# Performance work log

Measured on AMD Instinct MI355X. Metric: run time of the kernel, lower is better.

The kernel has to match this reference:

```python
import jax, jax.numpy as jnp
import numpy as np

N_TOKEN = 8192
N_EMBED = 512
N_SAMPLE = 10
TAU = 1.0
RHO = 1.0


def setup_inputs() -> dict:
    key = jax.random.key(0)
    k1, k2 = jax.random.split(key)
    inputs = jax.random.normal(k1, (4, 2048, N_EMBED), dtype=jnp.float32)
    embeds = jax.random.normal(k2, (N_TOKEN, N_EMBED), dtype=jnp.float32)
    return {"inputs": inputs, "embeds": embeds}


def reference(inputs, embeds):
    size = inputs.shape
    x = inputs.reshape(-1, N_EMBED)  # (N, D)
    n = x.shape[0]
    # squared distances, scaled by n_token (as in get_distances)
    dists = (jnp.sum(x * x, axis=-1, keepdims=True)
             + jnp.sum(embeds * embeds, axis=-1)[None, :]
             - 2.0 * jnp.matmul(x, embeds.T)) / N_TOKEN  # (N, K)
    logits = -dists / TAU  # categorical(softmax(logits)) == categorical(logits)
    skey = jax.random.fold_in(jax.random.key(0), 1)
    # multinomial with replacement: n_sample i.i.d. categorical draws per row
    samples = jax.random.categorical(skey, logits[:, None, :], axis=-1,
                                     shape=(n, N_SAMPLE))  # (N, n_sample) int
    quantized_embs = embeds[samples].mean(axis=1)  # (N, D) gather + mean
    quantized = x + jax.lax.stop_gradient(quantized_embs - x)  # straight-through
    gkey = jax.random.fold_in(jax.random.key(0), 2)
    gates = jax.random.bernoulli(gkey, RHO, (n,)).astype(x.dtype)[:, None]
    quantized = quantized * gates + (1.0 - gates) * x
    quantized = quantized.reshape(size)
    samples = samples.reshape(size[:-1] + (N_SAMPLE,))
    return quantized, samples
```

## Files before the change

kernel.cpp:

```cpp
#include <hip/hip_runtime.h>
#include <stdint.h>
#include <math.h>

#define N_ROWS 8192
#define N_TOK  8192
#define N_DIM  512
#define N_SAMP 10
#define GK     1536

typedef __attribute__((ext_vector_type(8))) short bf16x8_t;
typedef __attribute__((ext_vector_type(4))) float f32x4_t;

__host__ __device__ __forceinline__ void tf2x32(uint32_t ks0, uint32_t ks1,
                                                uint32_t& x0, uint32_t& x1) {
  uint32_t ks2 = ks0 ^ ks1 ^ 0x1BD11BDAu;
  x0 += ks0; x1 += ks1;
#define TF_ROUND(r) { x0 += x1; x1 = (x1 << (r)) | (x1 >> (32 - (r))); x1 ^= x0; }
  TF_ROUND(13) TF_ROUND(15) TF_ROUND(26) TF_ROUND(6)
  x0 += ks1; x1 += ks2 + 1u;
  TF_ROUND(17) TF_ROUND(29) TF_ROUND(16) TF_ROUND(24)
  x0 += ks2; x1 += ks0 + 2u;
  TF_ROUND(13) TF_ROUND(15) TF_ROUND(26) TF_ROUND(6)
  x0 += ks0; x1 += ks1 + 3u;
  TF_ROUND(17) TF_ROUND(29) TF_ROUND(16) TF_ROUND(24)
  x0 += ks1; x1 += ks2 + 4u;
  TF_ROUND(13) TF_ROUND(15) TF_ROUND(26) TF_ROUND(6)
  x0 += ks2; x1 += ks0 + 5u;
#undef TF_ROUND
}

__device__ __forceinline__ unsigned short f2bf_rne(float f) {
  uint32_t u = __float_as_uint(f);
  uint32_t r = (u + 0x7fffu + ((u >> 16) & 1u)) >> 16;
  return (unsigned short)r;
}
__device__ __forceinline__ float bf2f(unsigned short h) {
  return __uint_as_float((uint32_t)h << 16);
}

__global__ __launch_bounds__(256) void rownorm_kernel(const float* __restrict__ M,
                                                      float* __restrict__ out) {
  int lane = threadIdx.x & 63;
  int row = (int)((blockIdx.x * blockDim.x + threadIdx.x) >> 6);
  const float* p = M + (size_t)row * N_DIM;
  float acc = 0.f;
#pragma unroll
  for (int d = 0; d < N_DIM; d += 64) {
    float v = p[d + lane];
    acc = fmaf(v, v, acc);
  }
#pragma unroll
  for (int off = 32; off; off >>= 1) acc += __shfl_xor(acc, off, 64);
  if (lane == 0) out[row] = acc;
}

__global__ __launch_bounds__(256) void init_state_kernel(float* __restrict__ rmin,
                                                         int* __restrict__ ridx) {
  int i = blockIdx.x * 256 + threadIdx.x;
  if (i < N_ROWS * N_SAMP) { rmin[i] = INFINITY; ridx[i] = 0; }
}

__global__ __launch_bounds__(256) void split_kernel(const float* __restrict__ src,
                                                    unsigned short* __restrict__ dst,
                                                    int mode) {
  int t = blockIdx.x * 256 + threadIdx.x;
  int row = t >> 7;
  int c = (t & 127) << 2;
  float4 v = *(const float4*)(src + (size_t)row * N_DIM + c);
  ushort4 hi, lo;
  hi.x = f2bf_rne(v.x); lo.x = f2bf_rne(v.x - bf2f(hi.x));
  hi.y = f2bf_rne(v.y); lo.y = f2bf_rne(v.y - bf2f(hi.y));
  hi.z = f2bf_rne(v.z); lo.z = f2bf_rne(v.z - bf2f(hi.z));
  hi.w = f2bf_rne(v.w); lo.w = f2bf_rne(v.w - bf2f(hi.w));
  unsigned short* base = dst + (size_t)row * GK;
  *(ushort4*)(base + c) = hi;
  if (mode == 0) {
    *(ushort4*)(base + 512 + c) = lo;
    *(ushort4*)(base + 1024 + c) = hi;
  } else {
    *(ushort4*)(base + 512 + c) = hi;
    *(ushort4*)(base + 1024 + c) = lo;
  }
}

__device__ __forceinline__ void async_cp16(const void* g, void* l) {
  __builtin_amdgcn_global_load_lds((const __attribute__((address_space(1))) void*)g,
                                   (__attribute__((address_space(3))) void*)l, 16, 0, 0);
}

__global__ __launch_bounds__(256) void gemm_bf16_kernel(const unsigned short* __restrict__ A2,
                                                        const unsigned short* __restrict__ B2,
                                                        const float* __restrict__ xx,
                                                        const float* __restrict__ ee,
                                                        float* __restrict__ E,
                                                        int ks, int KC) {
  __shared__ __align__(16) unsigned short As[128 * 32];
  __shared__ __align__(16) unsigned short Bs[128 * 32];
  int tid = threadIdx.x;
  int w = tid >> 6, l = tid & 63;
  int row0 = blockIdx.y * 128;
  int col0 = blockIdx.x * 128;
  int bcol0 = ks + col0;
  int wm = (w & 1) * 64, wn = (w >> 1) * 64;
  int quad = l >> 4, r15 = l & 15;

  f32x4_t acc[4][4];
#pragma unroll
  for (int i = 0; i < 4; ++i)
#pragma unroll
    for (int j = 0; j < 4; ++j) acc[i][j] = (f32x4_t){0.f, 0.f, 0.f, 0.f};

  int c0 = w * 64 + l;
  int c1 = c0 + 256;
  const size_t ga0 = (size_t)(row0 + (c0 >> 2)) * GK + (c0 & 3) * 8;
  const size_t ga1 = (size_t)(row0 + (c1 >> 2)) * GK + (c1 & 3) * 8;
  const size_t gb0 = (size_t)(bcol0 + (c0 >> 2)) * GK + (c0 & 3) * 8;
  const size_t gb1 = (size_t)(bcol0 + (c1 >> 2)) * GK + (c1 & 3) * 8;

  for (int k0 = 0; k0 < GK; k0 += 32) {
    async_cp16(A2 + ga0 + k0, As + c0 * 8);
    async_cp16(A2 + ga1 + k0, As + c1 * 8);
    async_cp16(B2 + gb0 + k0, Bs + c0 * 8);
    async_cp16(B2 + gb1 + k0, Bs + c1 * 8);
    __syncthreads();

    bf16x8_t af[4], bf[4];
#pragma unroll
    for (int i = 0; i < 4; ++i)
      af[i] = *(const bf16x8_t*)&As[(wm + i * 16 + r15) * 32 + quad * 8];
#pragma unroll
    for (int j = 0; j < 4; ++j)
      bf[j] = *(const bf16x8_t*)&Bs[(wn + j * 16 + r15) * 32 + quad * 8];
#pragma unroll
    for (int i = 0; i < 4; ++i)
#pragma unroll
      for (int j = 0; j < 4; ++j)
        acc[i][j] = __builtin_amdgcn_mfma_f32_16x16x32_bf16(af[i], bf[j], acc[i][j], 0, 0, 0);
    __syncthreads();
  }

  const float inv_nt = 1.f / 8192.f;
  float eev[4];
#pragma unroll
  for (int j = 0; j < 4; ++j) eev[j] = ee[ks + col0 + wn + j * 16 + r15];
#pragma unroll
  for (int i = 0; i < 4; ++i) {
#pragma unroll
    for (int r = 0; r < 4; ++r) {
      int grow = row0 + wm + i * 16 + quad * 4 + r;
      float xxv = xx[grow];
#pragma unroll
      for (int j = 0; j < 4; ++j) {
        int gcol = col0 + wn + j * 16 + r15;
        float dist = (xxv + eev[j] - 2.0f * acc[i][j][r]) * inv_nt;
        E[(size_t)grow * KC + gcol] = expf(dist);
      }
    }
  }
}

__global__ __launch_bounds__(256) void gemm_nt_kernel(const float* __restrict__ A,
                                                      const float* __restrict__ B,
                                                      const float* __restrict__ xx,
                                                      const float* __restrict__ ee,
                                                      float* __restrict__ E,
                                                      int ks, int KC) {
  __shared__ __align__(16) float Asf[32][68];
  __shared__ __align__(16) float Bsf[32][68];
  int tid = threadIdx.x;
  int row0 = blockIdx.y * 64;
  int colB0 = blockIdx.x * 64 + ks;
  int tx = tid & 15, ty = tid >> 4;
  float acc[4][4] = {};
  for (int d0 = 0; d0 < N_DIM; d0 += 32) {
#pragma unroll
    for (int r = 0; r < 2; ++r) {
      int c = tid + 256 * r;
      int m = c >> 3;
      int dv = (c & 7) << 2;
      const float4 va = *(const float4*)(A + (size_t)(row0 + m) * N_DIM + d0 + dv);
      Asf[dv + 0][m] = va.x; Asf[dv + 1][m] = va.y;
      Asf[dv + 2][m] = va.z; Asf[dv + 3][m] = va.w;
      const float4 vb = *(const float4*)(B + (size_t)(colB0 + m) * N_DIM + d0 + dv);
      Bsf[dv + 0][m] = vb.x; Bsf[dv + 1][m] = vb.y;
      Bsf[dv + 2][m] = vb.z; Bsf[dv + 3][m] = vb.w;
    }
    __syncthreads();
#pragma unroll
    for (int dd = 0; dd < 32; ++dd) {
      float4 a4 = *(const float4*)&Asf[dd][ty << 2];
      float4 b4 = *(const float4*)&Bsf[dd][tx << 2];
      float av[4] = {a4.x, a4.y, a4.z, a4.w};
      float bv[4] = {b4.x, b4.y, b4.z, b4.w};
#pragma unroll
      for (int i = 0; i < 4; ++i)
#pragma unroll
        for (int j = 0; j < 4; ++j)
          acc[i][j] = fmaf(av[i], bv[j], acc[i][j]);
    }
    __syncthreads();
  }
  const float inv_nt = 1.f / 8192.f;
  int colC0 = blockIdx.x * 64;
  float eev[4];
#pragma unroll
  for (int j = 0; j < 4; ++j) eev[j] = ee[ks + colC0 + (tx << 2) + j];
#pragma unroll
  for (int i = 0; i < 4; ++i) {
    int grow = row0 + (ty << 2) + i;
    float xxv = xx[grow];
    float4 v;
    v.x = expf((xxv + eev[0] - 2.0f * acc[i][0]) * inv_nt);
    v.y = expf((xxv + eev[1] - 2.0f * acc[i][1]) * inv_nt);
    v.z = expf((xxv + eev[2] - 2.0f * acc[i][2]) * inv_nt);
    v.w = expf((xxv + eev[3] - 2.0f * acc[i][3]) * inv_nt);
    *(float4*)(E + (size_t)grow * KC + colC0 + (tx << 2)) = v;
  }
}

__global__ __launch_bounds__(256) void sample_kernel(const float* __restrict__ E,
                                                     float* __restrict__ rmin,
                                                     int* __restrict__ ridx,
                                                     int ks, int KC,
                                                     uint32_t k0, uint32_t k1) {
  int lane = threadIdx.x & 63;
  int row = (int)((blockIdx.x * blockDim.x + threadIdx.x) >> 6);
  float bmin[N_SAMP];
  int bidx[N_SAMP];
#pragma unroll
  for (int s = 0; s < N_SAMP; ++s) { bmin[s] = INFINITY; bidx[s] = 0; }
  const float tiny = 1.1754943508222875e-38f;
  uint32_t row_c = (uint32_t)row * (uint32_t)N_SAMP * 8192u;

  for (int kk = lane; kk < KC; kk += 64) {
    int k = ks + kk;
    float Ek = E[(size_t)row * KC + kk];
    uint32_t base_c = row_c + (uint32_t)k;
#pragma unroll
    for (int s = 0; s < N_SAMP; ++s) {
      uint32_t x0 = 0u, x1 = base_c + (uint32_t)s * 8192u;
      tf2x32(k0, k1, x0, x1);
      uint32_t bits = x0 ^ x1;
      float u = __uint_as_float(0x3f800000u | (bits >> 9)) - 1.0f;
      u = fmaxf(u, tiny);
      float wv = -logf(u) * Ek;
      if (wv < bmin[s]) { bmin[s] = wv; bidx[s] = k; }
    }
  }
#pragma unroll
  for (int s = 0; s < N_SAMP; ++s) {
    float v = bmin[s];
    int id = bidx[s];
#pragma unroll
    for (int off = 32; off; off >>= 1) {
      float ov = __shfl_xor(v, off, 64);
      int oi = __shfl_xor(id, off, 64);
      if (ov < v || (ov == v && oi < id)) { v = ov; id = oi; }
    }
    if (lane == 0) {
      size_t p = (size_t)row * N_SAMP + s;
      if (v < rmin[p]) { rmin[p] = v; ridx[p] = id; }
    }
  }
}

__global__ __launch_bounds__(256) void gather_kernel(const float* __restrict__ emb,
                                                     const int* __restrict__ ridx,
                                                     const float* __restrict__ x,
                                                     float* __restrict__ outq,
                                                     float* __restrict__ outs) {
  int lane = threadIdx.x & 63;
  int row = (int)((blockIdx.x * blockDim.x + threadIdx.x) >> 6);
  int idx[N_SAMP];
#pragma unroll
  for (int s = 0; s < N_SAMP; ++s) idx[s] = ridx[row * N_SAMP + s];
  if (lane < N_SAMP) outs[row * N_SAMP + lane] = (float)idx[lane];
#pragma unroll
  for (int c = lane; c < N_DIM; c += 64) {
    float sum = 0.f;
#pragma unroll
    for (int s = 0; s < N_SAMP; ++s) sum += emb[(size_t)idx[s] * N_DIM + c];
    float qe = sum / 10.0f;
    float xv = x[(size_t)row * N_DIM + c];
    outq[(size_t)row * N_DIM + c] = xv + (qe - xv);
  }
}

extern "C" void kernel_launch(void* const* d_in, const int* in_sizes, int n_in,
                              void* d_out, int out_size, void* d_ws, size_t ws_size,
                              hipStream_t stream) {
  const float* x = (const float*)d_in[0];
  const float* emb = (const float*)d_in[1];
  float* out_q = (float*)d_out;
  float* out_s = out_q + (size_t)N_ROWS * N_DIM;

  const size_t fixed_f = (size_t)N_ROWS + N_TOK + 2 * (size_t)N_ROWS * N_SAMP;
  const size_t out_f = (size_t)N_ROWS * N_DIM + (size_t)N_ROWS * N_SAMP;
  const size_t split_u = (size_t)N_ROWS * GK;

  uint32_t s0 = 0u, s1 = 1u;
  tf2x32(0u, 0u, s0, s1);

  int KC = 0;
  for (int c = 8192; c >= 128; c >>= 1) {
    size_t need = fixed_f * 4 + 2 * split_u * 2 + (size_t)N_ROWS * c * 4;
    if (need <= ws_size) { KC = c; break; }
  }

  if (KC) {
    float* xx = (float*)d_ws;
    float* ee = xx + N_ROWS;
    float* rmin = ee + N_TOK;
    int* ridx = (int*)(rmin + (size_t)N_ROWS * N_SAMP);
    unsigned short* A2 = (unsigned short*)(ridx + (size_t)N_ROWS * N_SAMP);
    unsigned short* B2 = A2 + split_u;
    float* E = (float*)(B2 + split_u);

    rownorm_kernel<<<2048, 256, 0, stream>>>(x, xx);
    rownorm_kernel<<<2048, 256, 0, stream>>>(emb, ee);
    init_state_kernel<<<(N_ROWS * N_SAMP + 255) / 256, 256, 0, stream>>>(rmin, ridx);
    split_kernel<<<N_ROWS * 128 / 256, 256, 0, stream>>>(x, A2, 0);
    split_kernel<<<N_ROWS * 128 / 256, 256, 0, stream>>>(emb, B2, 1);

    for (int ks = 0; ks < N_TOK; ks += KC) {
      gemm_bf16_kernel<<<dim3(KC / 128, N_ROWS / 128), 256, 0, stream>>>(A2, B2, xx, ee, E, ks, KC);
      sample_kernel<<<2048, 256, 0, stream>>>(E, rmin, ridx, ks, KC, s0, s1);
    }
    gather_kernel<<<2048, 256, 0, stream>>>(emb, ridx, x, out_q, out_s);
    return;
  }

  float *xx, *ee, *rmin, *E;
  int* ridx;
  KC = 0;
  for (int c = 8192; c >= 64; c >>= 1) {
    if ((fixed_f + (size_t)N_ROWS * c) * 4 <= ws_size) { KC = c; break; }
  }
  if (KC) {
    xx = (float*)d_ws;
    ee = xx + N_ROWS;
    rmin = ee + N_TOK;
    ridx = (int*)(rmin + (size_t)N_ROWS * N_SAMP);
    E = (float*)(ridx + (size_t)N_ROWS * N_SAMP);
  } else if (fixed_f * 4 <= ws_size) {
    KC = 512;
    xx = (float*)d_ws;
    ee = xx + N_ROWS;
    rmin = ee + N_TOK;
    ridx = (int*)(rmin + (size_t)N_ROWS * N_SAMP);
    E = out_q;
  } else {
    KC = 256;
    E = out_q;
    float* tail = out_q + (out_f - fixed_f);
    xx = tail;
    ee = xx + N_ROWS;
    rmin = ee + N_TOK;
    ridx = (int*)(rmin + (size_t)N_ROWS * N_SAMP);
  }

  rownorm_kernel<<<2048, 256, 0, stream>>>(x, xx);
  rownorm_kernel<<<2048, 256, 0, stream>>>(emb, ee);
  init_state_kernel<<<(N_ROWS * N_SAMP + 255) / 256, 256, 0, stream>>>(rmin, ridx);
  for (int ks = 0; ks < N_TOK; ks += KC) {
    gemm_nt_kernel<<<dim3(KC / 64, N_ROWS / 64), 256, 0, stream>>>(x, emb, xx, ee, E, ks, KC);
    sample_kernel<<<2048, 256, 0, stream>>>(E, rmin, ridx, ks, KC, s0, s1);
  }
  gather_kernel<<<2048, 256, 0, stream>>>(emb, ridx, x, out_q, out_s);
}
```

Before: 1.724 ms.

## Deepen GEMM K-tile, swizzle block order, prune sampling log, vectorize gather

The bf16 GEMM now loads 64-wide K tiles per barrier and remaps block indices into bands of 8 row-tiles for better L2 reuse. The sampling kernel keeps a running per-sample wave-wide champion and a uniform threshold, so logf and the wave reduction run only when some lane could beat the current minimum. The gather kernel uses float4 loads and stores. The threshold pruning adds per-iteration ballots and shuffles, and its correctness depends on the threshold bound being conservative.

```diff
diff --git a/kernel.cpp b/kernel.cpp
--- a/kernel.cpp
+++ b/kernel.cpp
@@ -36,6 +36,13 @@
 }
 __device__ __forceinline__ float bf2f(unsigned short h) {
   return __uint_as_float((uint32_t)h << 16);
+}
+
+__device__ __forceinline__ unsigned long long shfl_xor_u64(unsigned long long v, int off) {
+  uint32_t lo = (uint32_t)v, hi = (uint32_t)(v >> 32);
+  lo = (uint32_t)__shfl_xor((int)lo, off, 64);
+  hi = (uint32_t)__shfl_xor((int)hi, off, 64);
+  return ((unsigned long long)hi << 32) | lo;
 }
 
 __global__ __launch_bounds__(256) void rownorm_kernel(const float* __restrict__ M,
@@ -94,12 +101,20 @@
                                                         const float* __restrict__ ee,
                                                         float* __restrict__ E,
                                                         int ks, int KC) {
-  __shared__ __align__(16) unsigned short As[128 * 32];
-  __shared__ __align__(16) unsigned short Bs[128 * 32];
+  __shared__ __align__(16) unsigned short As[128 * 64];
+  __shared__ __align__(16) unsigned short Bs[128 * 64];
   int tid = threadIdx.x;
   int w = tid >> 6, l = tid & 63;
-  int row0 = blockIdx.y * 128;
-  int col0 = blockIdx.x * 128;
+
+  int gx = gridDim.x;
+  int bid = blockIdx.y * gx + blockIdx.x;
+  int band = bid / (8 * gx);
+  int t8 = bid % (8 * gx);
+  int by = band * 8 + (t8 & 7);
+  int bx = t8 >> 3;
+
+  int row0 = by * 128;
+  int col0 = bx * 128;
   int bcol0 = ks + col0;
   int wm = (w & 1) * 64, wn = (w >> 1) * 64;
   int quad = l >> 4, r15 = l & 15;
@@ -110,32 +125,31 @@
 #pragma unroll
     for (int j = 0; j < 4; ++j) acc[i][j] = (f32x4_t){0.f, 0.f, 0.f, 0.f};
 
-  int c0 = w * 64 + l;
-  int c1 = c0 + 256;
-  const size_t ga0 = (size_t)(row0 + (c0 >> 2)) * GK + (c0 & 3) * 8;
-  const size_t ga1 = (size_t)(row0 + (c1 >> 2)) * GK + (c1 & 3) * 8;
-  const size_t gb0 = (size_t)(bcol0 + (c0 >> 2)) * GK + (c0 & 3) * 8;
-  const size_t gb1 = (size_t)(bcol0 + (c1 >> 2)) * GK + (c1 & 3) * 8;
-
-  for (int k0 = 0; k0 < GK; k0 += 32) {
-    async_cp16(A2 + ga0 + k0, As + c0 * 8);
-    async_cp16(A2 + ga1 + k0, As + c1 * 8);
-    async_cp16(B2 + gb0 + k0, Bs + c0 * 8);
-    async_cp16(B2 + gb1 + k0, Bs + c1 * 8);
+  for (int k0 = 0; k0 < GK; k0 += 64) {
+#pragma unroll
+    for (int r = 0; r < 4; ++r) {
+      int c = tid + 256 * r;
+      int rw = c >> 3, kc = c & 7;
+      async_cp16(A2 + (size_t)(row0 + rw) * GK + k0 + kc * 8, As + c * 8);
+      async_cp16(B2 + (size_t)(bcol0 + rw) * GK + k0 + kc * 8, Bs + c * 8);
+    }
     __syncthreads();
 
-    bf16x8_t af[4], bf[4];
-#pragma unroll
-    for (int i = 0; i < 4; ++i)
-      af[i] = *(const bf16x8_t*)&As[(wm + i * 16 + r15) * 32 + quad * 8];
-#pragma unroll
-    for (int j = 0; j < 4; ++j)
-      bf[j] = *(const bf16x8_t*)&Bs[(wn + j * 16 + r15) * 32 + quad * 8];
-#pragma unroll
-    for (int i = 0; i < 4; ++i)
+#pragma unroll
+    for (int kk2 = 0; kk2 < 2; ++kk2) {
+      bf16x8_t af[4], bf[4];
+#pragma unroll
+      for (int i = 0; i < 4; ++i)
+        af[i] = *(const bf16x8_t*)&As[(wm + i * 16 + r15) * 64 + kk2 * 32 + quad * 8];
 #pragma unroll
       for (int j = 0; j < 4; ++j)
-        acc[i][j] = __builtin_amdgcn_mfma_f32_16x16x32_bf16(af[i], bf[j], acc[i][j], 0, 0, 0);
+        bf[j] = *(const bf16x8_t*)&Bs[(wn + j * 16 + r15) * 64 + kk2 * 32 + quad * 8];
+#pragma unroll
+      for (int i = 0; i < 4; ++i)
+#pragma unroll
+        for (int j = 0; j < 4; ++j)
+          acc[i][j] = __builtin_amdgcn_mfma_f32_16x16x32_bf16(af[i], bf[j], acc[i][j], 0, 0, 0);
+    }
     __syncthreads();
   }
 
@@ -225,39 +239,49 @@
                                                      uint32_t k0, uint32_t k1) {
   int lane = threadIdx.x & 63;
   int row = (int)((blockIdx.x * blockDim.x + threadIdx.x) >> 6);
-  float bmin[N_SAMP];
-  int bidx[N_SAMP];
-#pragma unroll
-  for (int s = 0; s < N_SAMP; ++s) { bmin[s] = INFINITY; bidx[s] = 0; }
+  unsigned long long champ[N_SAMP];
+  uint32_t th[N_SAMP];
+#pragma unroll
+  for (int s = 0; s < N_SAMP; ++s) { champ[s] = 0xFFFFFFFFFFFFFFFFULL; th[s] = 0u; }
   const float tiny = 1.1754943508222875e-38f;
-  uint32_t row_c = (uint32_t)row * (uint32_t)N_SAMP * 8192u;
+  uint32_t row_c = (uint32_t)row * 81920u;
 
   for (int kk = lane; kk < KC; kk += 64) {
-    int k = ks + kk;
+    uint32_t k = (uint32_t)(ks + kk);
     float Ek = E[(size_t)row * KC + kk];
-    uint32_t base_c = row_c + (uint32_t)k;
+    uint32_t base_c = row_c + k;
 #pragma unroll
     for (int s = 0; s < N_SAMP; ++s) {
       uint32_t x0 = 0u, x1 = base_c + (uint32_t)s * 8192u;
       tf2x32(k0, k1, x0, x1);
       uint32_t bits = x0 ^ x1;
-      float u = __uint_as_float(0x3f800000u | (bits >> 9)) - 1.0f;
-      u = fmaxf(u, tiny);
-      float wv = -logf(u) * Ek;
-      if (wv < bmin[s]) { bmin[s] = wv; bidx[s] = k; }
+      bool cand = (bits >= th[s]);
+      if (__any(cand)) {
+        float u = __uint_as_float(0x3f800000u | (bits >> 9)) - 1.0f;
+        u = fmaxf(u, tiny);
+        float wv = -logf(u) * Ek;
+        unsigned long long p = cand
+            ? (((unsigned long long)__float_as_uint(wv) << 32) | k)
+            : 0xFFFFFFFFFFFFFFFFULL;
+#pragma unroll
+        for (int off = 1; off < 64; off <<= 1) {
+          unsigned long long op = shfl_xor_u64(p, off);
+          p = (op < p) ? op : p;
+        }
+        if (p < champ[s]) {
+          champ[s] = p;
+          float wmin = __uint_as_float((uint32_t)(p >> 32));
+          float ut = expf(-wmin) * 0.999999f;
+          th[s] = ((uint32_t)(ut * 8388608.0f)) << 9;
+        }
+      }
     }
   }
 #pragma unroll
   for (int s = 0; s < N_SAMP; ++s) {
-    float v = bmin[s];
-    int id = bidx[s];
-#pragma unroll
-    for (int off = 32; off; off >>= 1) {
-      float ov = __shfl_xor(v, off, 64);
-      int oi = __shfl_xor(id, off, 64);
-      if (ov < v || (ov == v && oi < id)) { v = ov; id = oi; }
-    }
     if (lane == 0) {
+      float v = __uint_as_float((uint32_t)(champ[s] >> 32));
+      int id = (int)(uint32_t)(champ[s] & 0xFFFFFFFFu);
       size_t p = (size_t)row * N_SAMP + s;
       if (v < rmin[p]) { rmin[p] = v; ridx[p] = id; }
     }
@@ -276,13 +300,21 @@
   for (int s = 0; s < N_SAMP; ++s) idx[s] = ridx[row * N_SAMP + s];
   if (lane < N_SAMP) outs[row * N_SAMP + lane] = (float)idx[lane];
 #pragma unroll
-  for (int c = lane; c < N_DIM; c += 64) {
-    float sum = 0.f;
-#pragma unroll
-    for (int s = 0; s < N_SAMP; ++s) sum += emb[(size_t)idx[s] * N_DIM + c];
-    float qe = sum / 10.0f;
-    float xv = x[(size_t)row * N_DIM + c];
-    outq[(size_t)row * N_DIM + c] = xv + (qe - xv);
+  for (int h = 0; h < 2; ++h) {
+    int c = h * 256 + lane * 4;
+    float4 sum = make_float4(0.f, 0.f, 0.f, 0.f);
+#pragma unroll
+    for (int s = 0; s < N_SAMP; ++s) {
+      float4 e = *(const float4*)(emb + (size_t)idx[s] * N_DIM + c);
+      sum.x += e.x; sum.y += e.y; sum.z += e.z; sum.w += e.w;
+    }
+    float4 xv = *(const float4*)(x + (size_t)row * N_DIM + c);
+    float4 o;
+    o.x = xv.x + (sum.x / 10.0f - xv.x);
+    o.y = xv.y + (sum.y / 10.0f - xv.y);
+    o.z = xv.z + (sum.z / 10.0f - xv.z);
+    o.w = xv.w + (sum.w / 10.0f - xv.w);
+    *(float4*)(outq + (size_t)row * N_DIM + c) = o;
   }
 }
 
```

After: 1.702 ms. About the same (-1.3%).
